# Kernel optimization log

Hardware: AMD Instinct MI355X
Metric: run time of the kernel (lower is better)

## Reference

```python
import jax, jax.numpy as jnp
import numpy as np

B, H, T = 32, 48, 24
S, A, R, F, L = 256, 64, 8, 1024, 2
EPS = 1e-5


def setup_inputs() -> dict:
    key = jax.random.key(0)
    ks = jax.random.split(key, 12)
    def w(k, shape):
        fan_in = shape[-1]
        return jax.random.normal(k, shape, jnp.float32) / jnp.sqrt(jnp.float32(fan_in))
    return {
        'history_s': jax.random.normal(ks[0], (B, H, S), jnp.float32),
        'history_a': jax.random.normal(ks[1], (B, H, A), jnp.float32),
        'present_s': jax.random.normal(ks[2], (B, S), jnp.float32),
        'future_s': jax.random.normal(ks[3], (B, T, S), jnp.float32),
        'future_a': jax.random.normal(ks[4], (B, T, A), jnp.float32),
        'W_state': w(ks[5], (F, S)), 'b_state': jnp.zeros((F,), jnp.float32),
        'g_sn': jnp.ones((F,), jnp.float32), 'b_sn': jnp.zeros((F,), jnp.float32),
        'W_action': w(ks[6], (F, A)), 'b_action': jnp.zeros((F,), jnp.float32),
        'g_an': jnp.ones((F,), jnp.float32), 'b_an': jnp.zeros((F,), jnp.float32),
        'gru_Wi': w(ks[7], (L, 3 * F, F)), 'gru_Wh': w(ks[8], (L, 3 * F, F)),
        'gru_bi': jnp.zeros((L, 3 * F), jnp.float32), 'gru_bh': jnp.zeros((L, 3 * F), jnp.float32),
        'W_reward': w(ks[9], (R, F)), 'b_reward': jnp.zeros((R,), jnp.float32),
        'W_sout': w(ks[10], (S, F)), 'b_sout': jnp.zeros((S,), jnp.float32),
    }


def _ln(x, g, b):
    m = jnp.mean(x, axis=-1, keepdims=True)
    v = jnp.mean(jnp.square(x - m), axis=-1, keepdims=True)
    return (x - m) / jnp.sqrt(v + EPS) * g + b


def _gelu(x):
    return jax.nn.gelu(x, approximate=False)  # torch F.gelu default = exact erf


def _gru_step(Wi, Wh, bi, bh, hs, x):
    # hs: [L,B,F] hidden per layer; x: [B,F]. PyTorch GRU cell semantics.
    new_hs = []
    inp = x
    for l in range(Wi.shape[0]):
        gi = inp @ Wi[l].T + bi[l]      # [B,3F]
        gh = hs[l] @ Wh[l].T + bh[l]    # [B,3F]
        ir, iz, inn = jnp.split(gi, 3, axis=-1)
        hr, hz, hn = jnp.split(gh, 3, axis=-1)
        r = jax.nn.sigmoid(ir + hr)
        z = jax.nn.sigmoid(iz + hz)
        n = jnp.tanh(inn + r * hn)
        h_new = (1.0 - z) * n + z * hs[l]
        new_hs.append(h_new)
        inp = h_new  # dropout between layers is identity (drop_rate=0)
    return jnp.stack(new_hs), inp


def reference(history_s, history_a, present_s, future_s, future_a,
              W_state, b_state, g_sn, b_sn, W_action, b_action, g_an, b_an,
              gru_Wi, gru_Wh, gru_bi, gru_bh, W_reward, b_reward, W_sout, b_sout):
    # Original forward() reruns the GRU from scratch over a growing window each
    # future step; since h0=0 this is mathematically identical to carrying the
    # hidden state incrementally (module's own _forward variant), which we do.
    Bv = history_s.shape[0]
    Fv = W_state.shape[0]
    Lv = gru_Wi.shape[0]

    hs = _ln(history_s @ W_state.T + b_state, g_sn, b_sn)   # [B,H,F]
    ha = _ln(history_a @ W_action.T + b_action, g_an, b_an)  # [B,H,F]
    ps = _ln(present_s @ W_state.T + b_state, g_sn, b_sn)    # [B,F]
    fa = _ln(future_a @ W_action.T + b_action, g_an, b_an)   # [B,T,F]

    hist_sa = hs + ha  # [B,H,F]

    def head(y):
        r = jnp.tanh(y @ W_reward.T + b_reward)
        s = y @ W_sout.T + b_sout  # state_activation is identity
        return r, s

    # step 0: full window = history + (present + future_a[0])
    seq0 = _gelu(jnp.concatenate([hist_sa, (ps + fa[:, 0])[:, None, :]], axis=1))
    h0 = jnp.zeros((Lv, Bv, Fv), seq0.dtype)

    def scan_seq(h, x):
        h, y = _gru_step(gru_Wi, gru_Wh, gru_bi, gru_bh, h, x)
        return h, y

    hT, ys = jax.lax.scan(scan_seq, h0, jnp.swapaxes(seq0, 0, 1))  # ys: [H+1,B,F]
    r0, s0 = head(ys[-1])
    pres = _ln(s0 @ W_state.T + b_state, g_sn, b_sn)

    def scan_fut(carry, fa_t):
        h, p = carry
        x = _gelu(p + fa_t)  # [B,F]
        h, y = _gru_step(gru_Wi, gru_Wh, gru_bi, gru_bh, h, x)
        r, s = head(y)
        p_new = _ln(s @ W_state.T + b_state, g_sn, b_sn)
        return (h, p_new), (r, s)

    _, (rs, ss) = jax.lax.scan(scan_fut, (hT, pres), jnp.swapaxes(fa[:, 1:], 0, 1))
    future_r = jnp.concatenate([r0[:, None], jnp.swapaxes(rs, 0, 1)], axis=1)  # [B,T,R]
    future_s_out = jnp.concatenate([s0[:, None], jnp.swapaxes(ss, 0, 1)], axis=1)  # [B,T,S]
    return future_r, future_s_out
```

## Files before the change

kernel.cpp:

```cpp
#include <hip/hip_runtime.h>
#include <cmath>

constexpr int kB = 32, kH = 48, kT = 24, kS = 256, kA = 64, kR = 8, kF = 1024;
constexpr int kSEQ = kH + 1;
constexpr float kEPS = 1e-5f;

constexpr int G  = 128;
constexpr int BT = 512;

typedef __attribute__((ext_vector_type(8))) short short8;
typedef __attribute__((ext_vector_type(4))) float f32x4;

union U4S8 { uint4 u; short8 s; };

__device__ __forceinline__ unsigned bfbits(float x) {
  unsigned u = __float_as_uint(x);
  return (u + 0x7fffu + ((u >> 16) & 1u)) >> 16;
}
__device__ __forceinline__ float bf_lo(unsigned u) { return __uint_as_float(u << 16); }
__device__ __forceinline__ float bf_hi(unsigned u) { return __uint_as_float(u & 0xffff0000u); }
__device__ __forceinline__ float bf2f(unsigned short h) {
  return __uint_as_float(((unsigned)h) << 16);
}
__device__ __forceinline__ float gelu_f(float x) {
  return 0.5f * x * (1.0f + erff(x * 0.7071067811865476f));
}
__device__ __forceinline__ float sigmoid_f(float x) {
  return 1.0f / (1.0f + expf(-x));
}

__device__ __forceinline__ void coh_st(unsigned* p, unsigned v) {
  __hip_atomic_store(p, v, __ATOMIC_RELAXED, __HIP_MEMORY_SCOPE_AGENT);
}

__device__ __forceinline__ void wwait(const unsigned* line, unsigned tgt) {
  for (;;) {
    unsigned v;
    asm volatile("global_load_dword %0, %1, off sc0 sc1\n\t"
                 "s_waitcnt vmcnt(0)"
                 : "=v"(v) : "v"(line) : "memory");
    if (v >= tgt) break;
    __builtin_amdgcn_s_sleep(1);
  }
}
__device__ __forceinline__ void wait4(const unsigned* fl,
                                      unsigned t0, unsigned t1,
                                      unsigned t2, unsigned t3) {
  if (threadIdx.x == 0) {
    for (;;) {
      unsigned a, b, c, d;
      asm volatile(
        "global_load_dword %0, %4, off sc0 sc1\n\t"
        "global_load_dword %1, %5, off sc0 sc1\n\t"
        "global_load_dword %2, %6, off sc0 sc1\n\t"
        "global_load_dword %3, %7, off sc0 sc1\n\t"
        "s_waitcnt vmcnt(0)"
        : "=&v"(a), "=&v"(b), "=&v"(c), "=&v"(d)
        : "v"(fl), "v"(fl + 32), "v"(fl + 64), "v"(fl + 96)
        : "memory");
      if (a >= t0 && b >= t1 && c >= t2 && d >= t3) break;
      __builtin_amdgcn_s_sleep(1);
    }
  }
  __syncthreads();
}
__device__ __forceinline__ void sig_oct(unsigned* fl, int fb) {
  if (threadIdx.x == 0)
    __hip_atomic_fetch_add(fl + ((fb >> 3) & 7) * 32, 1u,
                           __ATOMIC_RELAXED, __HIP_MEMORY_SCOPE_AGENT);
}
__device__ __forceinline__ void sig16(unsigned* fl, int b) {
  if (threadIdx.x == 0)
    __hip_atomic_fetch_add(fl + ((b >> 4) & 1) * 32, 1u,
                           __ATOMIC_RELAXED, __HIP_MEMORY_SCOPE_AGENT);
}

__device__ __forceinline__ void layer_stage(
    const unsigned short* __restrict__ xsrc,
    const unsigned short* __restrict__ hsrc,
    unsigned short* __restrict__ hdst,
    const unsigned* xw8,
    const unsigned* hw8,
    const unsigned* xblk2,
    int hfirst,
    const short8 (&Bf)[2][3][4],
    float bR, float bZ, float bIN, float bHN,
    float& h_old, float* part, int fb)
{
  const int tid = threadIdx.x;
  const int wv = tid >> 6, l = tid & 63, q = l >> 4, c = l & 15;

  short8 Ax[2][4], Ah[2][4];
  const int base = c*1024 + wv*128 + q*8;

  if (hfirst) {
    if (hw8) wwait(hw8 + wv*32, 8u);
    #pragma unroll
    for (int mt = 0; mt < 2; mt++)
      #pragma unroll
      for (int j = 0; j < 4; j++)
        Ah[mt][j] = *(const short8*)(hsrc + base + mt*16*1024 + j*32);
    if (xblk2) wait4(xblk2, 16u, 16u, 0u, 0u);
    if (xw8) wwait(xw8 + wv*32, 8u);
    #pragma unroll
    for (int mt = 0; mt < 2; mt++)
      #pragma unroll
      for (int j = 0; j < 4; j++)
        Ax[mt][j] = *(const short8*)(xsrc + base + mt*16*1024 + j*32);
  } else {
    #pragma unroll
    for (int mt = 0; mt < 2; mt++)
      #pragma unroll
      for (int j = 0; j < 4; j++)
        Ax[mt][j] = *(const short8*)(xsrc + base + mt*16*1024 + j*32);
    if (hw8) wwait(hw8 + wv*32, 8u);
    #pragma unroll
    for (int mt = 0; mt < 2; mt++)
      #pragma unroll
      for (int j = 0; j < 4; j++)
        Ah[mt][j] = *(const short8*)(hsrc + base + mt*16*1024 + j*32);
  }

  f32x4 C[4][2];
  #pragma unroll
  for (int s = 0; s < 4; s++)
    #pragma unroll
    for (int mt = 0; mt < 2; mt++)
      C[s][mt] = (f32x4){0.f, 0.f, 0.f, 0.f};

  #pragma unroll
  for (int mt = 0; mt < 2; mt++)
    #pragma unroll
    for (int j = 0; j < 4; j++) {
      C[0][mt] = __builtin_amdgcn_mfma_f32_16x16x32_bf16(Ax[mt][j], Bf[0][0][j], C[0][mt], 0, 0, 0);
      C[0][mt] = __builtin_amdgcn_mfma_f32_16x16x32_bf16(Ah[mt][j], Bf[1][0][j], C[0][mt], 0, 0, 0);
      C[1][mt] = __builtin_amdgcn_mfma_f32_16x16x32_bf16(Ax[mt][j], Bf[0][1][j], C[1][mt], 0, 0, 0);
      C[1][mt] = __builtin_amdgcn_mfma_f32_16x16x32_bf16(Ah[mt][j], Bf[1][1][j], C[1][mt], 0, 0, 0);
      C[2][mt] = __builtin_amdgcn_mfma_f32_16x16x32_bf16(Ax[mt][j], Bf[0][2][j], C[2][mt], 0, 0, 0);
      C[3][mt] = __builtin_amdgcn_mfma_f32_16x16x32_bf16(Ah[mt][j], Bf[1][2][j], C[3][mt], 0, 0, 0);
    }

  const int perm = (wv + l + (l >> 3)) & 7;
  #pragma unroll
  for (int s = 0; s < 4; s++)
    #pragma unroll
    for (int mt = 0; mt < 2; mt++)
      #pragma unroll
      for (int r = 0; r < 4; r++)
        part[((s*2 + mt)*4 + r)*512 + l*8 + perm] = C[s][mt][r];
  __syncthreads();

  const int mt_c = wv & 1, rg = wv >> 1;
  const int b_own = mt_c*16 + q*4 + rg;
  float S[4];
  #pragma unroll
  for (int s = 0; s < 4; s++) {
    const float* pp = part + ((s*2 + mt_c)*4 + rg)*512 + l*8;
    f32x4 a = *(const f32x4*)pp;
    f32x4 b = *(const f32x4*)(pp + 4);
    S[s] = ((a[0]+a[1]) + (a[2]+a[3])) + ((b[0]+b[1]) + (b[2]+b[3]));
  }
  float rr = sigmoid_f(S[0] + bR);
  float zz = sigmoid_f(S[1] + bZ);
  float nn = tanhf(S[2] + bIN + rr * (S[3] + bHN));
  float hn = (1.f - zz)*nn + zz*h_old;
  h_old = hn;
  float nb = __shfl_xor(hn, 1);
  if (!(c & 1)) {
    unsigned pk = bfbits(hn) | (bfbits(nb) << 16);
    coh_st((unsigned*)(hdst + b_own*1024 + fb*16 + c), pk);
  }
  __syncthreads();
}

__device__ __forceinline__ void f3_stage(
    const unsigned short* __restrict__ y_bf, int t,
    const unsigned short* __restrict__ WsT2_bf, const float* __restrict__ b_sout,
    const unsigned short* __restrict__ Wr_bf, const float* __restrict__ b_reward,
    const unsigned short* __restrict__ WstT_bf, const float* __restrict__ b_state,
    const float* __restrict__ g_sn, const float* __restrict__ b_sn,
    const unsigned short* __restrict__ fa_bf,
    float* __restrict__ out_r, float* __restrict__ out_s,
    unsigned short* __restrict__ xbuf_bf, float* part, int b)
{
  const int tid = threadIdx.x;
  float* yb    = part;
  float* spart = part + 1024;
  float* s_sh  = part + 1536;
  float* rpart = part + 1792;
  float* red1  = part + 2048;
  float* red2  = part + 2560;

  {
    unsigned uu = *((const unsigned*)y_bf + b*512 + tid);
    yb[tid*2]     = bf_lo(uu);
    yb[tid*2 + 1] = bf_hi(uu);
  }
  __syncthreads();
  {
    const int j = tid & 255, ksh = tid >> 8;
    const unsigned* wp = (const unsigned*)WsT2_bf + (size_t)ksh*256*256 + j;
    const float* yp = yb + ksh*512;
    float acc = 0.f;
    #pragma unroll 8
    for (int kp = 0; kp < 256; kp++) {
      unsigned w = wp[kp*256];
      acc += bf_lo(w)*yp[2*kp] + bf_hi(w)*yp[2*kp + 1];
    }
    spart[tid] = acc;
  }
  __syncthreads();
  if (tid < 256) {
    float s = spart[tid] + spart[tid + 256] + b_sout[tid];
    out_s[((size_t)b*kT + t)*kS + tid] = s;
    s_sh[tid] = s;
  } else if (tid < 320) {
    const int idx = tid - 256, j = idx >> 3, ks = idx & 7;
    const unsigned short* wr = Wr_bf + j*1024 + ks*128;
    const float* yp = yb + ks*128;
    float acc = 0.f;
    #pragma unroll 4
    for (int k = 0; k < 128; k += 2) {
      unsigned w = *(const unsigned*)(wr + k);
      acc += bf_lo(w)*yp[k] + bf_hi(w)*yp[k+1];
    }
    rpart[idx] = acc;
  }
  __syncthreads();
  if (tid < 8) {
    float a = b_reward[tid];
    #pragma unroll
    for (int ks = 0; ks < 8; ks++) a += rpart[tid*8 + ks];
    out_r[((size_t)b*kT + t)*kR + tid] = tanhf(a);
  }
  if (t == kT - 1) return;
  __syncthreads();
  const int f0 = tid*2;
  float a0 = b_state[f0], a1 = b_state[f0 + 1];
  {
    const unsigned* wp = (const unsigned*)WstT_bf + (f0 >> 1);
    #pragma unroll 8
    for (int k = 0; k < 256; k++) {
      unsigned w = wp[k*512];
      a0 += bf_lo(w)*s_sh[k];
      a1 += bf_hi(w)*s_sh[k];
    }
  }
  float s1 = a0 + a1, s2 = a0*a0 + a1*a1;
  red1[tid] = s1; red2[tid] = s2;
  __syncthreads();
  for (int off = 256; off > 0; off >>= 1) {
    if (tid < off) { red1[tid] += red1[tid + off]; red2[tid] += red2[tid + off]; }
    __syncthreads();
  }
  const float mean = red1[0] * (1.0f/kF);
  const float var  = red2[0] * (1.0f/kF) - mean*mean;
  const float inv  = rsqrtf(var + kEPS);
  unsigned fu = *((const unsigned*)(fa_bf + ((size_t)(t+1)*kB + b)*kF) + tid);
  float x0 = (a0 - mean)*inv*g_sn[f0]   + b_sn[f0]   + bf_lo(fu);
  float x1 = (a1 - mean)*inv*g_sn[f0+1] + b_sn[f0+1] + bf_hi(fu);
  unsigned pk = bfbits(gelu_f(x0)) | (bfbits(gelu_f(x1)) << 16);
  coh_st((unsigned*)xbuf_bf + b*512 + tid, pk);
}

__device__ __forceinline__ void load_bfrags(
    const float* __restrict__ gru_Wi, const float* __restrict__ gru_Wh,
    int lay, int fb, int wv, int q, int c, short8 (&Bf)[2][3][4])
{
  const size_t WLL = (size_t)3 * kF * kF;
  const float* Wm[2] = { gru_Wi + lay*WLL, gru_Wh + lay*WLL };
  #pragma unroll
  for (int m = 0; m < 2; m++)
    #pragma unroll
    for (int g = 0; g < 3; g++)
      #pragma unroll
      for (int j = 0; j < 4; j++) {
        const float* p = Wm[m] + ((size_t)(g*kF + fb*16 + c))*kF + wv*128 + j*32 + q*8;
        float4 a = *(const float4*)p;
        float4 b = *(const float4*)(p + 4);
        U4S8 u;
        u.u.x = bfbits(a.x) | (bfbits(a.y) << 16);
        u.u.y = bfbits(a.z) | (bfbits(a.w) << 16);
        u.u.z = bfbits(b.x) | (bfbits(b.y) << 16);
        u.u.w = bfbits(b.z) | (bfbits(b.w) << 16);
        Bf[m][g][j] = u.s;
      }
}

__global__ __launch_bounds__(BT, 2) void gru_hist(
    const float* __restrict__ gru_Wi, const float* __restrict__ gru_Wh,
    const float* __restrict__ gru_bi, const float* __restrict__ gru_bh,
    const unsigned short* __restrict__ seq0_bf,
    unsigned short* h0pool, unsigned short* h1pool,
    unsigned* hflags)
{
  __shared__ float part[32 * 512];
  const int tid = threadIdx.x;
  const int blk = blockIdx.x;
  const int wv = tid >> 6, l = tid & 63, q = l >> 4, c = l & 15;
  const bool isL1 = (blk >= 64);
  const int fb = blk & 63;
  const int lay = isL1 ? 1 : 0;
  const size_t BF = (size_t)kB * kF;

  short8 Bf[2][3][4];
  load_bfrags(gru_Wi, gru_Wh, lay, fb, wv, q, c, Bf);
  const int f = fb*16 + c;
  const float* bi = gru_bi + lay*3*kF;
  const float* bh = gru_bh + lay*3*kF;
  const float bR  = bi[f] + bh[f];
  const float bZ  = bi[kF + f] + bh[kF + f];
  const float bIN = bi[2*kF + f];
  const float bHN = bh[2*kF + f];

  float h_old = 0.f;

  #define H0P(i) (h0pool + (size_t)(i)*BF)
  #define H1P(i) (h1pool + (size_t)(i)*BF)
  #define FH0(s) (hflags + (size_t)((s) - 1) * 256)
  #define FH1(s) (hflags + (size_t)(48 + (s)) * 256)

  for (int s = 0; s < 50; s++) {
    if (!isL1) {
      if (s < 49) {
        layer_stage(seq0_bf + (size_t)s*BF, H0P(s), H0P(s+1),
                    nullptr, (s >= 1) ? FH0(s) : nullptr, nullptr, 0,
                    Bf, bR, bZ, bIN, bHN, h_old, part, fb);
        sig_oct(FH0(s+1), fb);
      }
    } else {
      if (s >= 1) {
        layer_stage(H0P(s), H1P(s-1), H1P(s),
                    FH0(s), (s >= 2) ? FH1(s-1) : nullptr, nullptr, 1,
                    Bf, bR, bZ, bIN, bHN, h_old, part, fb);
        sig_oct(FH1(s), fb);
      }
    }
  }
  #undef H0P
  #undef H1P
  #undef FH0
  #undef FH1
}

__global__ __launch_bounds__(BT, 2) void gru_fut(
    const float* __restrict__ gru_Wi, const float* __restrict__ gru_Wh,
    const float* __restrict__ gru_bi, const float* __restrict__ gru_bh,
    const unsigned short* __restrict__ WsT2_bf, const float* __restrict__ b_sout,
    const unsigned short* __restrict__ Wr_bf, const float* __restrict__ b_reward,
    const unsigned short* __restrict__ WstT_bf, const float* __restrict__ b_state,
    const float* __restrict__ g_sn, const float* __restrict__ b_sn,
    const unsigned short* __restrict__ fa_bf,
    unsigned short* h0pool, unsigned short* h1pool, unsigned short* xbpool,
    unsigned* fflags,
    float* __restrict__ out_r, float* __restrict__ out_s)
{
  __shared__ float part[32 * 512];
  const int tid = threadIdx.x;
  const int blk = blockIdx.x;
  const int wv = tid >> 6, l = tid & 63, q = l >> 4, c = l & 15;
  const bool isL1 = (blk >= 64);
  const int fb = blk & 63;
  const int lay = isL1 ? 1 : 0;
  const size_t BF = (size_t)kB * kF;

  short8 Bf[2][3][4];
  load_bfrags(gru_Wi, gru_Wh, lay, fb, wv, q, c, Bf);
  const int f = fb*16 + c;
  const float* bi = gru_bi + lay*3*kF;
  const float* bh = gru_bh + lay*3*kF;
  const float bR  = bi[f] + bh[f];
  const float bZ  = bi[kF + f] + bh[kF + f];
  const float bIN = bi[2*kF + f];
  const float bHN = bh[2*kF + f];

  #define H0P(i) (h0pool + (size_t)(i)*BF)
  #define H1P(i) (h1pool + (size_t)(i)*BF)
  #define XBP(i) (xbpool + (size_t)(i)*BF)
  #define FH0F(t) (fflags + (size_t)(t) * 256)
  #define FH1F(t) (fflags + (size_t)(23 + (t)) * 256)
  #define FXF(t)  (fflags + (size_t)46 * 256 + (size_t)(t) * 64)

  const int b_own = (wv & 1)*16 + q*4 + (wv >> 1);
  float h_old;
  {
    const unsigned short* hs = isL1 ? H1P(49) : H0P(49);
    h_old = bf2f(hs[b_own*1024 + f]);
  }

  for (int t = 0; t < kT; t++) {
    if (blk < kB) {
      if (t >= 1) {
        wait4(FH1F(t-1), 8u, 8u, 8u, 8u);
        wait4(FH1F(t-1) + 128, 8u, 8u, 8u, 8u);
      }
      f3_stage(H1P(49+t), t, WsT2_bf, b_sout, Wr_bf, b_reward,
               WstT_bf, b_state, g_sn, b_sn, fa_bf,
               out_r, out_s, XBP(t), part, blk);
      if (t < kT - 1) { __syncthreads(); sig16(FXF(t), blk); }
    }
    if (t == kT - 1) break;
    if (!isL1) {
      layer_stage(XBP(t), H0P(49+t), H0P(50+t),
                  nullptr, (t >= 1) ? FH0F(t-1) : nullptr, FXF(t), 1,
                  Bf, bR, bZ, bIN, bHN, h_old, part, fb);
      sig_oct(FH0F(t), fb);
    } else {
      layer_stage(H0P(50+t), H1P(49+t), H1P(50+t),
                  FH0F(t), (t >= 1) ? FH1F(t-1) : nullptr, nullptr, 1,
                  Bf, bR, bZ, bIN, bHN, h_old, part, fb);
      sig_oct(FH1F(t), fb);
    }
  }
  #undef H0P
  #undef H1P
  #undef XBP
  #undef FH0F
  #undef FH1F
  #undef FXF
}

__global__ __launch_bounds__(512) void convert_weights(
    const float* __restrict__ ws,  unsigned short* __restrict__ wsT2,
    const float* __restrict__ wst, unsigned short* __restrict__ wstT,
    const float* __restrict__ wr,  unsigned short* __restrict__ o3)
{
  const int stride = gridDim.x * blockDim.x;
  const int i0 = blockIdx.x * blockDim.x + threadIdx.x;
  for (int i = i0; i < kS*kF; i += stride) {
    const int j = i >> 10, k = i & 1023;
    wsT2[(k >> 1)*512 + j*2 + (k & 1)] = (unsigned short)bfbits(ws[i]);
  }
  for (int i = i0; i < kF*kS; i += stride) {
    const int ff = i >> 8, k = i & 255;
    wstT[k*1024 + ff] = (unsigned short)bfbits(wst[i]);
  }
  for (int i = i0; i < kR*kF; i += stride) o3[i] = (unsigned short)bfbits(wr[i]);
}

__global__ __launch_bounds__(256) void encode_fa_kernel(
    const float* __restrict__ future_a,
    const float* __restrict__ W_action, const float* __restrict__ b_action,
    const float* __restrict__ g_an, const float* __restrict__ b_an,
    unsigned short* __restrict__ fa_bf)
{
  __shared__ __align__(16) float arow[kA];
  __shared__ float red1[256], red2[256];
  const int bid = blockIdx.x;
  const int b = bid & (kB - 1);
  const int t = bid >> 5;
  const int tid = threadIdx.x;
  if (tid < kA) arow[tid] = future_a[((size_t)b*kT + t)*kA + tid];
  __syncthreads();
  float v[4]; float s1 = 0.f, s2 = 0.f;
  #pragma unroll
  for (int j = 0; j < 4; j++) {
    const int ff = tid + j*256;
    const float* wr = W_action + (size_t)ff*kA;
    float acc = b_action[ff];
    for (int k = 0; k < kA; k += 4) {
      float4 w  = *(const float4*)(wr + k);
      float4 xv = *(const float4*)(arow + k);
      acc += xv.x*w.x + xv.y*w.y + xv.z*w.z + xv.w*w.w;
    }
    v[j] = acc; s1 += acc; s2 += acc*acc;
  }
  red1[tid] = s1; red2[tid] = s2;
  __syncthreads();
  for (int off = 128; off > 0; off >>= 1) {
    if (tid < off) { red1[tid] += red1[tid+off]; red2[tid] += red2[tid+off]; }
    __syncthreads();
  }
  const float m = red1[0] * (1.0f/kF);
  const float va = red2[0] * (1.0f/kF) - m*m;
  const float inv = rsqrtf(va + kEPS);
  #pragma unroll
  for (int j = 0; j < 4; j++) {
    const int ff = tid + j*256;
    fa_bf[((size_t)t*kB + b)*kF + ff] =
        (unsigned short)bfbits((v[j] - m)*inv*g_an[ff] + b_an[ff]);
  }
}

__global__ __launch_bounds__(256) void encode_seq0_kernel(
    const float* __restrict__ history_s, const float* __restrict__ history_a,
    const float* __restrict__ present_s,
    const float* __restrict__ W_state, const float* __restrict__ b_state,
    const float* __restrict__ g_sn, const float* __restrict__ b_sn,
    const float* __restrict__ W_action, const float* __restrict__ b_action,
    const float* __restrict__ g_an, const float* __restrict__ b_an,
    const unsigned short* __restrict__ fa_bf, unsigned short* __restrict__ seq0_bf)
{
  __shared__ __align__(16) float srow[kS];
  __shared__ __align__(16) float arow[kA];
  __shared__ float red1[256], red2[256];
  const int bid = blockIdx.x;
  const int b = bid & (kB - 1);
  const int t = bid >> 5;
  const int tid = threadIdx.x;
  const bool hist = (t < kH);
  const float* sp = hist ? (history_s + ((size_t)b*kH + t)*kS)
                         : (present_s + (size_t)b*kS);
  srow[tid] = sp[tid];
  if (hist && tid < kA) arow[tid] = history_a[((size_t)b*kH + t)*kA + tid];
  __syncthreads();

  float u[4]; float s1 = 0.f, s2 = 0.f;
  #pragma unroll
  for (int j = 0; j < 4; j++) {
    const int ff = tid + j*256;
    const float* wr = W_state + (size_t)ff*kS;
    float acc = b_state[ff];
    for (int k = 0; k < kS; k += 4) {
      float4 w  = *(const float4*)(wr + k);
      float4 xv = *(const float4*)(srow + k);
      acc += xv.x*w.x + xv.y*w.y + xv.z*w.z + xv.w*w.w;
    }
    u[j] = acc; s1 += acc; s2 += acc*acc;
  }
  red1[tid] = s1; red2[tid] = s2;
  __syncthreads();
  for (int off = 128; off > 0; off >>= 1) {
    if (tid < off) { red1[tid] += red1[tid+off]; red2[tid] += red2[tid+off]; }
    __syncthreads();
  }
  const float mu = red1[0] * (1.0f/kF);
  const float vu = red2[0] * (1.0f/kF) - mu*mu;
  const float iu = rsqrtf(vu + kEPS);
  __syncthreads();

  if (hist) {
    float v[4]; s1 = 0.f; s2 = 0.f;
    #pragma unroll
    for (int j = 0; j < 4; j++) {
      const int ff = tid + j*256;
      const float* wr = W_action + (size_t)ff*kA;
      float acc = b_action[ff];
      for (int k = 0; k < kA; k += 4) {
        float4 w  = *(const float4*)(wr + k);
        float4 xv = *(const float4*)(arow + k);
        acc += xv.x*w.x + xv.y*w.y + xv.z*w.z + xv.w*w.w;
      }
      v[j] = acc; s1 += acc; s2 += acc*acc;
    }
    red1[tid] = s1; red2[tid] = s2;
    __syncthreads();
    for (int off = 128; off > 0; off >>= 1) {
      if (tid < off) { red1[tid] += red1[tid+off]; red2[tid] += red2[tid+off]; }
      __syncthreads();
    }
    const float mv = red1[0] * (1.0f/kF);
    const float vv = red2[0] * (1.0f/kF) - mv*mv;
    const float iv = rsqrtf(vv + kEPS);
    #pragma unroll
    for (int j = 0; j < 4; j++) {
      const int ff = tid + j*256;
      const float un = (u[j] - mu)*iu*g_sn[ff] + b_sn[ff];
      const float vn = (v[j] - mv)*iv*g_an[ff] + b_an[ff];
      seq0_bf[((size_t)t*kB + b)*kF + ff] = (unsigned short)bfbits(gelu_f(un + vn));
    }
  } else {
    #pragma unroll
    for (int j = 0; j < 4; j++) {
      const int ff = tid + j*256;
      const float un = (u[j] - mu)*iu*g_sn[ff] + b_sn[ff];
      seq0_bf[((size_t)t*kB + b)*kF + ff] =
          (unsigned short)bfbits(gelu_f(un + bf2f(fa_bf[(size_t)b*kF + ff])));
    }
  }
}

extern "C" void kernel_launch(void* const* d_in, const int* in_sizes, int n_in,
                              void* d_out, int out_size, void* d_ws, size_t ws_size,
                              hipStream_t stream) {
  (void)in_sizes; (void)n_in; (void)out_size;
  const float* history_s = (const float*)d_in[0];
  const float* history_a = (const float*)d_in[1];
  const float* present_s = (const float*)d_in[2];
  const float* future_a  = (const float*)d_in[4];
  const float* W_state   = (const float*)d_in[5];
  const float* b_state   = (const float*)d_in[6];
  const float* g_sn      = (const float*)d_in[7];
  const float* b_sn      = (const float*)d_in[8];
  const float* W_action  = (const float*)d_in[9];
  const float* b_action  = (const float*)d_in[10];
  const float* g_an      = (const float*)d_in[11];
  const float* b_an      = (const float*)d_in[12];
  const float* gru_Wi    = (const float*)d_in[13];
  const float* gru_Wh    = (const float*)d_in[14];
  const float* gru_bi    = (const float*)d_in[15];
  const float* gru_bh    = (const float*)d_in[16];
  const float* W_reward  = (const float*)d_in[17];
  const float* b_reward  = (const float*)d_in[18];
  const float* W_sout    = (const float*)d_in[19];
  const float* b_sout    = (const float*)d_in[20];

  char* ws = (char*)d_ws;
  unsigned short* seq0_bf = (unsigned short*)(ws + 0);
  unsigned short* fa_bf   = (unsigned short*)(ws + 3211264);
  unsigned short* WsT2_bf = (unsigned short*)(ws + 4784128);
  unsigned short* WstT_bf = (unsigned short*)(ws + 5308416);
  unsigned short* Wr_bf   = (unsigned short*)(ws + 5832704);
  unsigned short* h0pool  = (unsigned short*)(ws + 5849088);
  unsigned short* h1pool  = (unsigned short*)(ws + 10633216);
  unsigned short* xbpool  = (unsigned short*)(ws + 15417344);
  unsigned*       hflags  = (unsigned*)(ws + 16924672);
  unsigned*       fflags  = (unsigned*)(ws + 17025024);
  const size_t need = 17078016;
  if (ws_size < need) return;

  hipMemsetAsync((void*)h0pool, 0, 65536, stream);
  hipMemsetAsync((void*)h1pool, 0, 65536, stream);
  hipMemsetAsync((void*)hflags, 0, 100352 + 52992, stream);

  float* out_r = (float*)d_out;
  float* out_s = out_r + (size_t)kB*kT*kR;

  hipLaunchKernelGGL(convert_weights, dim3(256), dim3(512), 0, stream,
                     W_sout, WsT2_bf, W_state, WstT_bf, W_reward, Wr_bf);
  hipLaunchKernelGGL(encode_fa_kernel, dim3(kT*kB), dim3(256), 0, stream,
                     future_a, W_action, b_action, g_an, b_an, fa_bf);
  hipLaunchKernelGGL(encode_seq0_kernel, dim3(kSEQ*kB), dim3(256), 0, stream,
                     history_s, history_a, present_s,
                     W_state, b_state, g_sn, b_sn,
                     W_action, b_action, g_an, b_an, fa_bf, seq0_bf);
  hipLaunchKernelGGL(gru_hist, dim3(G), dim3(BT), 0, stream,
                     gru_Wi, gru_Wh, gru_bi, gru_bh,
                     seq0_bf, h0pool, h1pool, hflags);
  hipLaunchKernelGGL(gru_fut, dim3(G), dim3(BT), 0, stream,
                     gru_Wi, gru_Wh, gru_bi, gru_bh,
                     WsT2_bf, b_sout, Wr_bf, b_reward, WstT_bf, b_state,
                     g_sn, b_sn, fa_bf,
                     h0pool, h1pool, xbpool, fflags,
                     out_r, out_s);
}
```

Before: 1.472 ms.

## Move output heads off recurrent critical path and add MFMA heater blocks

```diff
diff --git a/kernel.cpp b/kernel.cpp
--- a/kernel.cpp
+++ b/kernel.cpp
@@ -6,6 +6,7 @@
 constexpr float kEPS = 1e-5f;
 
 constexpr int G  = 128;
+constexpr int GH = 192;
 constexpr int BT = 512;
 
 typedef __attribute__((ext_vector_type(8))) short short8;
@@ -28,11 +29,27 @@
 __device__ __forceinline__ float sigmoid_f(float x) {
   return 1.0f / (1.0f + expf(-x));
 }
+__device__ __forceinline__ float dot8bb(const unsigned short* w, const unsigned short* y) {
+  uint4 a = *(const uint4*)w; uint4 b = *(const uint4*)y;
+  float r = 0.f;
+  r += bf_lo(a.x)*bf_lo(b.x); r += bf_hi(a.x)*bf_hi(b.x);
+  r += bf_lo(a.y)*bf_lo(b.y); r += bf_hi(a.y)*bf_hi(b.y);
+  r += bf_lo(a.z)*bf_lo(b.z); r += bf_hi(a.z)*bf_hi(b.z);
+  r += bf_lo(a.w)*bf_lo(b.w); r += bf_hi(a.w)*bf_hi(b.w);
+  return r;
+}
 
 __device__ __forceinline__ void coh_st(unsigned* p, unsigned v) {
   __hip_atomic_store(p, v, __ATOMIC_RELAXED, __HIP_MEMORY_SCOPE_AGENT);
 }
 
+__device__ __forceinline__ unsigned poll_ld(const unsigned* p) {
+  unsigned v;
+  asm volatile("global_load_dword %0, %1, off sc0 sc1\n\t"
+               "s_waitcnt vmcnt(0)"
+               : "=v"(v) : "v"(p) : "memory");
+  return v;
+}
 __device__ __forceinline__ void wwait(const unsigned* line, unsigned tgt) {
   for (;;) {
     unsigned v;
@@ -75,6 +92,26 @@
                            __ATOMIC_RELAXED, __HIP_MEMORY_SCOPE_AGENT);
 }
 
+__device__ __forceinline__ void heater_spin(const unsigned* done, int cap) {
+  __shared__ unsigned hstop;
+  if (threadIdx.x == 0) hstop = 0u;
+  __syncthreads();
+  f32x4 acc = (f32x4){0.f, 0.f, 0.f, 0.f};
+  short8 a = (short8){0, 0, 0, 0, 0, 0, 0, 0};
+  for (int i = 0; i < cap; i++) {
+    #pragma unroll
+    for (int j = 0; j < 8; j++)
+      acc = __builtin_amdgcn_mfma_f32_16x16x32_bf16(a, a, acc, 0, 0, 0);
+    if ((i & 511) == 511) {
+      if (threadIdx.x == 0) hstop = poll_ld(done);
+      __syncthreads();
+      if (hstop) break;
+      __syncthreads();
+    }
+  }
+  asm volatile("" :: "v"(acc[0]));
+}
+
 __device__ __forceinline__ void layer_stage(
     const unsigned short* __restrict__ xsrc,
     const unsigned short* __restrict__ hsrc,
@@ -176,18 +213,15 @@
 __device__ __forceinline__ void f3_stage(
     const unsigned short* __restrict__ y_bf, int t,
     const unsigned short* __restrict__ WsT2_bf, const float* __restrict__ b_sout,
-    const unsigned short* __restrict__ Wr_bf, const float* __restrict__ b_reward,
     const unsigned short* __restrict__ WstT_bf, const float* __restrict__ b_state,
     const float* __restrict__ g_sn, const float* __restrict__ b_sn,
     const unsigned short* __restrict__ fa_bf,
-    float* __restrict__ out_r, float* __restrict__ out_s,
     unsigned short* __restrict__ xbuf_bf, float* part, int b)
 {
   const int tid = threadIdx.x;
   float* yb    = part;
   float* spart = part + 1024;
   float* s_sh  = part + 1536;
-  float* rpart = part + 1792;
   float* red1  = part + 2048;
   float* red2  = part + 2560;
 
@@ -211,29 +245,8 @@
   }
   __syncthreads();
   if (tid < 256) {
-    float s = spart[tid] + spart[tid + 256] + b_sout[tid];
-    out_s[((size_t)b*kT + t)*kS + tid] = s;
-    s_sh[tid] = s;
-  } else if (tid < 320) {
-    const int idx = tid - 256, j = idx >> 3, ks = idx & 7;
-    const unsigned short* wr = Wr_bf + j*1024 + ks*128;
-    const float* yp = yb + ks*128;
-    float acc = 0.f;
-    #pragma unroll 4
-    for (int k = 0; k < 128; k += 2) {
-      unsigned w = *(const unsigned*)(wr + k);
-      acc += bf_lo(w)*yp[k] + bf_hi(w)*yp[k+1];
-    }
-    rpart[idx] = acc;
-  }
-  __syncthreads();
-  if (tid < 8) {
-    float a = b_reward[tid];
-    #pragma unroll
-    for (int ks = 0; ks < 8; ks++) a += rpart[tid*8 + ks];
-    out_r[((size_t)b*kT + t)*kR + tid] = tanhf(a);
-  }
-  if (t == kT - 1) return;
+    s_sh[tid] = spart[tid] + spart[tid + 256] + b_sout[tid];
+  }
   __syncthreads();
   const int f0 = tid*2;
   float a0 = b_state[f0], a1 = b_state[f0 + 1];
@@ -292,11 +305,12 @@
     const float* __restrict__ gru_bi, const float* __restrict__ gru_bh,
     const unsigned short* __restrict__ seq0_bf,
     unsigned short* h0pool, unsigned short* h1pool,
-    unsigned* hflags)
+    unsigned* hflags, unsigned* done)
 {
   __shared__ float part[32 * 512];
+  const int blk = blockIdx.x;
+  if (blk >= G) { heater_spin(done, 30000); return; }
   const int tid = threadIdx.x;
-  const int blk = blockIdx.x;
   const int wv = tid >> 6, l = tid & 63, q = l >> 4, c = l & 15;
   const bool isL1 = (blk >= 64);
   const int fb = blk & 63;
@@ -337,6 +351,7 @@
       }
     }
   }
+  if (blk == 127 && tid == 0) coh_st(done, 1u);
   #undef H0P
   #undef H1P
   #undef FH0
@@ -347,17 +362,19 @@
     const float* __restrict__ gru_Wi, const float* __restrict__ gru_Wh,
     const float* __restrict__ gru_bi, const float* __restrict__ gru_bh,
     const unsigned short* __restrict__ WsT2_bf, const float* __restrict__ b_sout,
+    const unsigned short* __restrict__ Ws_bf,
     const unsigned short* __restrict__ Wr_bf, const float* __restrict__ b_reward,
     const unsigned short* __restrict__ WstT_bf, const float* __restrict__ b_state,
     const float* __restrict__ g_sn, const float* __restrict__ b_sn,
     const unsigned short* __restrict__ fa_bf,
     unsigned short* h0pool, unsigned short* h1pool, unsigned short* xbpool,
-    unsigned* fflags,
+    unsigned* fflags, unsigned* done,
     float* __restrict__ out_r, float* __restrict__ out_s)
 {
   __shared__ float part[32 * 512];
+  const int blk = blockIdx.x;
+  if (blk >= G) { heater_spin(done, 30000); return; }
   const int tid = threadIdx.x;
-  const int blk = blockIdx.x;
   const int wv = tid >> 6, l = tid & 63, q = l >> 4, c = l & 15;
   const bool isL1 = (blk >= 64);
   const int fb = blk & 63;
@@ -388,18 +405,18 @@
     h_old = bf2f(hs[b_own*1024 + f]);
   }
 
-  for (int t = 0; t < kT; t++) {
+  for (int t = 0; t < kT - 1; t++) {
     if (blk < kB) {
       if (t >= 1) {
         wait4(FH1F(t-1), 8u, 8u, 8u, 8u);
         wait4(FH1F(t-1) + 128, 8u, 8u, 8u, 8u);
       }
-      f3_stage(H1P(49+t), t, WsT2_bf, b_sout, Wr_bf, b_reward,
+      f3_stage(H1P(49+t), t, WsT2_bf, b_sout,
                WstT_bf, b_state, g_sn, b_sn, fa_bf,
-               out_r, out_s, XBP(t), part, blk);
-      if (t < kT - 1) { __syncthreads(); sig16(FXF(t), blk); }
-    }
-    if (t == kT - 1) break;
+               XBP(t), part, blk);
+      __syncthreads();
+      sig16(FXF(t), blk);
+    }
     if (!isL1) {
       layer_stage(XBP(t), H0P(49+t), H0P(50+t),
                   nullptr, (t >= 1) ? FH0F(t-1) : nullptr, FXF(t), 1,
@@ -412,6 +429,78 @@
       sig_oct(FH1F(t), fb);
     }
   }
+
+  if (blk < 96) {
+    const int t = blk >> 2, jq = blk & 3;
+    if (t >= 1) {
+      wait4(FH1F(t-1), 8u, 8u, 8u, 8u);
+      wait4(FH1F(t-1) + 128, 8u, 8u, 8u, 8u);
+    } else {
+      __syncthreads();
+    }
+    const unsigned short* y = H1P(49 + t);
+    short8 Ay[2][4], Bs[4][4];
+    #pragma unroll
+    for (int j = 0; j < 4; j++) {
+      const int koff = wv*128 + j*32 + q*8;
+      Ay[0][j] = *(const short8*)(y + c*1024 + koff);
+      Ay[1][j] = *(const short8*)(y + (16 + c)*1024 + koff);
+      #pragma unroll
+      for (int g = 0; g < 4; g++)
+        Bs[g][j] = *(const short8*)(Ws_bf + (size_t)(jq*64 + g*16 + c)*1024 + koff);
+    }
+    f32x4 C[4][2];
+    #pragma unroll
+    for (int g = 0; g < 4; g++) {
+      C[g][0] = (f32x4){0.f,0.f,0.f,0.f};
+      C[g][1] = (f32x4){0.f,0.f,0.f,0.f};
+    }
+    #pragma unroll
+    for (int j = 0; j < 4; j++)
+      #pragma unroll
+      for (int g = 0; g < 4; g++) {
+        C[g][0] = __builtin_amdgcn_mfma_f32_16x16x32_bf16(Ay[0][j], Bs[g][j], C[g][0], 0, 0, 0);
+        C[g][1] = __builtin_amdgcn_mfma_f32_16x16x32_bf16(Ay[1][j], Bs[g][j], C[g][1], 0, 0, 0);
+      }
+    const int perm = (wv + l + (l >> 3)) & 7;
+    #pragma unroll
+    for (int g = 0; g < 4; g++)
+      #pragma unroll
+      for (int mt = 0; mt < 2; mt++)
+        #pragma unroll
+        for (int r = 0; r < 4; r++)
+          part[((g*2 + mt)*4 + r)*512 + l*8 + perm] = C[g][mt][r];
+    __syncthreads();
+    const int mt_c = wv & 1, rg = wv >> 1;
+    const int bo = mt_c*16 + q*4 + rg;
+    #pragma unroll
+    for (int g = 0; g < 4; g++) {
+      const float* pp = part + ((g*2 + mt_c)*4 + rg)*512 + l*8;
+      f32x4 a = *(const f32x4*)pp;
+      f32x4 b2 = *(const f32x4*)(pp + 4);
+      float S = ((a[0]+a[1]) + (a[2]+a[3])) + ((b2[0]+b2[1]) + (b2[2]+b2[3]));
+      const int col = jq*64 + g*16 + c;
+      out_s[((size_t)bo*kT + t)*kS + col] = S + b_sout[col];
+    }
+  } else if (blk < 96 + kT) {
+    const int t = blk - 96;
+    if (t >= 1) {
+      wait4(FH1F(t-1), 8u, 8u, 8u, 8u);
+      wait4(FH1F(t-1) + 128, 8u, 8u, 8u, 8u);
+    }
+    const unsigned short* y = H1P(49 + t);
+    const int idx = tid >> 1, half = tid & 1;
+    const int b = idx >> 3, j = idx & 7;
+    const unsigned short* wr = Wr_bf + j*1024 + half*512;
+    const unsigned short* yp = y + b*1024 + half*512;
+    float acc = 0.f;
+    #pragma unroll 8
+    for (int k = 0; k < 512; k += 8) acc += dot8bb(wr + k, yp + k);
+    acc += __shfl_xor(acc, 1);
+    if (half == 0)
+      out_r[((size_t)b*kT + t)*kR + j] = tanhf(acc + b_reward[j]);
+  }
+  if (blk == 127 && tid == 0) coh_st(done, 1u);
   #undef H0P
   #undef H1P
   #undef XBP
@@ -422,6 +511,7 @@
 
 __global__ __launch_bounds__(512) void convert_weights(
     const float* __restrict__ ws,  unsigned short* __restrict__ wsT2,
+    unsigned short* __restrict__ wsRow,
     const float* __restrict__ wst, unsigned short* __restrict__ wstT,
     const float* __restrict__ wr,  unsigned short* __restrict__ o3)
 {
@@ -429,7 +519,9 @@
   const int i0 = blockIdx.x * blockDim.x + threadIdx.x;
   for (int i = i0; i < kS*kF; i += stride) {
     const int j = i >> 10, k = i & 1023;
-    wsT2[(k >> 1)*512 + j*2 + (k & 1)] = (unsigned short)bfbits(ws[i]);
+    const unsigned short v = (unsigned short)bfbits(ws[i]);
+    wsT2[(k >> 1)*512 + j*2 + (k & 1)] = v;
+    wsRow[i] = v;
   }
   for (int i = i0; i < kF*kS; i += stride) {
     const int ff = i >> 8, k = i & 255;
@@ -600,37 +692,39 @@
   unsigned short* fa_bf   = (unsigned short*)(ws + 3211264);
   unsigned short* WsT2_bf = (unsigned short*)(ws + 4784128);
   unsigned short* WstT_bf = (unsigned short*)(ws + 5308416);
-  unsigned short* Wr_bf   = (unsigned short*)(ws + 5832704);
-  unsigned short* h0pool  = (unsigned short*)(ws + 5849088);
-  unsigned short* h1pool  = (unsigned short*)(ws + 10633216);
-  unsigned short* xbpool  = (unsigned short*)(ws + 15417344);
-  unsigned*       hflags  = (unsigned*)(ws + 16924672);
-  unsigned*       fflags  = (unsigned*)(ws + 17025024);
-  const size_t need = 17078016;
+  unsigned short* Ws_bf   = (unsigned short*)(ws + 5832704);
+  unsigned short* Wr_bf   = (unsigned short*)(ws + 6356992);
+  unsigned short* h0pool  = (unsigned short*)(ws + 6373376);
+  unsigned short* h1pool  = (unsigned short*)(ws + 11157504);
+  unsigned short* xbpool  = (unsigned short*)(ws + 15941632);
+  unsigned*       hflags  = (unsigned*)(ws + 17448960);
+  unsigned*       fflags  = (unsigned*)(ws + 17549312);
+  unsigned*       done    = (unsigned*)(ws + 17602304);
+  const size_t need = 17602560;
   if (ws_size < need) return;
 
   hipMemsetAsync((void*)h0pool, 0, 65536, stream);
   hipMemsetAsync((void*)h1pool, 0, 65536, stream);
-  hipMemsetAsync((void*)hflags, 0, 100352 + 52992, stream);
+  hipMemsetAsync((void*)hflags, 0, 100352 + 52992 + 256, stream);
 
   float* out_r = (float*)d_out;
   float* out_s = out_r + (size_t)kB*kT*kR;
 
   hipLaunchKernelGGL(convert_weights, dim3(256), dim3(512), 0, stream,
-                     W_sout, WsT2_bf, W_state, WstT_bf, W_reward, Wr_bf);
+                     W_sout, WsT2_bf, Ws_bf, W_state, WstT_bf, W_reward, Wr_bf);
   hipLaunchKernelGGL(encode_fa_kernel, dim3(kT*kB), dim3(256), 0, stream,
                      future_a, W_action, b_action, g_an, b_an, fa_bf);
   hipLaunchKernelGGL(encode_seq0_kernel, dim3(kSEQ*kB), dim3(256), 0, stream,
                      history_s, history_a, present_s,
                      W_state, b_state, g_sn, b_sn,
                      W_action, b_action, g_an, b_an, fa_bf, seq0_bf);
-  hipLaunchKernelGGL(gru_hist, dim3(G), dim3(BT), 0, stream,
+  hipLaunchKernelGGL(gru_hist, dim3(GH), dim3(BT), 0, stream,
                      gru_Wi, gru_Wh, gru_bi, gru_bh,
-                     seq0_bf, h0pool, h1pool, hflags);
-  hipLaunchKernelGGL(gru_fut, dim3(G), dim3(BT), 0, stream,
+                     seq0_bf, h0pool, h1pool, hflags, done);
+  hipLaunchKernelGGL(gru_fut, dim3(GH), dim3(BT), 0, stream,
                      gru_Wi, gru_Wh, gru_bi, gru_bh,
-                     WsT2_bf, b_sout, Wr_bf, b_reward, WstT_bf, b_state,
+                     WsT2_bf, b_sout, Ws_bf, Wr_bf, b_reward, WstT_bf, b_state,
                      g_sn, b_sn, fa_bf,
-                     h0pool, h1pool, xbpool, fflags,
+                     h0pool, h1pool, xbpool, fflags, done + 32,
                      out_r, out_s);
 }
```

New measurement: 1.518 ms. 3.1% more time.
